# Kernel tuning notes

Measured on AMD Instinct MI355X. Metric: run time of the kernel, lower is better.

## Reference

```python
import jax, jax.numpy as jnp
import numpy as np

N_BITS = 8
IN_FEATURES = 2048
OUT_FEATURES = 512
BATCH = 8
THRESHOLD = 0.5


def setup_inputs() -> dict:
    key = jax.random.key(0)
    kx, kw = jax.random.split(key)
    x = jax.random.uniform(kx, (BATCH, IN_FEATURES), dtype=jnp.float32)
    # nn.init.normal_(weight, mean=0.5, std=1.0) then clamp_(0, 1)
    weight = 0.5 + jax.random.normal(kw, (IN_FEATURES, OUT_FEATURES * N_BITS), dtype=jnp.float32)
    weight = jnp.clip(weight, 0.0, 1.0)
    return {"x": x, "weight": weight}


def _carry_save_adder(addends):
    # addends: [M, F, n_bits] -> reduce over F via full-adder chain.
    # Bit index 0 = LSB; carry shifts one position toward MSB each step.
    M, F, nb = addends.shape
    a_seq = jnp.transpose(addends, (1, 0, 2))  # [F, M, nb]
    init = (jnp.zeros((M, nb), addends.dtype), jnp.zeros((M, nb), addends.dtype))

    def step(state, a):
        s, c = state
        t = s + a + c
        half = jnp.floor(t * 0.5)          # carry bit (zero-gradient)
        sum_b = t - 2.0 * half             # t mod 2 (identity gradient w.r.t. t)
        c_next = jnp.pad(half[:, :-1], ((0, 0), (1, 0)))  # shift-left: LSB carry-in = 0
        return (sum_b, c_next), None

    (s, c), _ = jax.lax.scan(step, init, a_seq)
    return s, c


def reference(x, weight):
    # STE binarization of the weights (forward value = hard bits)
    w = jnp.clip(weight, 0.0, 1.0)
    hard = w + jax.lax.stop_gradient((w >= THRESHOLD).astype(w.dtype) - w)
    # [B, F, 1] * [1, F, O*nb] -> [B, F, O*nb]
    ff = x[:, :, None] * hard[None, :, :]
    B, F, _ = ff.shape
    O = ff.shape[-1] // N_BITS
    # split(n_bits, dim=-1) + stack(dim=-3) + reshape -> [B*O, F, n_bits]
    stacked = ff.reshape(B, F, O, N_BITS).transpose(0, 2, 1, 3).reshape(B * O, F, N_BITS)
    s, carry = _carry_save_adder(stacked)   # [B*O, nb], [B*O, nb]
    s = s.reshape(B, N_BITS * O)
    return (s, carry)
```

## Files before the change

### kernel.cpp

```cpp
#include <hip/hip_runtime.h>


#define F_DIM 2048
#define K_DIM 4096
#define B_DIM 8
#define G     32
#define NG    (F_DIM / G)
#define NSB   (F_DIM / 64)

#define PK_BYTES (64 * NG * 64 * 4)

__device__ __forceinline__ float dpp_row_shr1(float v) {
    int r = __builtin_amdgcn_update_dpp(0, __float_as_int(v), 0x111, 0xf, 0xf, true);
    return __int_as_float(r);
}

__device__ __forceinline__ int sext_bit(unsigned bits, int u) {
#if __has_builtin(__builtin_amdgcn_sbfe)
    return __builtin_amdgcn_sbfe((int)bits, (unsigned)u, 1u);
#else
    return ((int)(bits << (31 - u))) >> 31;
#endif
}

__global__ __launch_bounds__(64) void pack_kernel(const float* __restrict__ w,
                                                  unsigned* __restrict__ pk) {
    const int lane = threadIdx.x;
    const int og   = blockIdx.x;
    const int f32  = blockIdx.y;
    const float* wp = w + og * 64 + lane;
    unsigned bits = 0;
#pragma unroll
    for (int j = 0; j < 32; ++j) {
        float wv = wp[(f32 * 32 + j) * K_DIM];
        bits |= (wv >= 0.5f ? 1u : 0u) << j;
    }
    pk[(og * 64 + f32) * 64 + lane] = bits;
}

__global__ __launch_bounds__(64, 1) void csa_main(const float* __restrict__ x,
                                                  const unsigned* __restrict__ pk,
                                                  float* __restrict__ out) {
    const int lane = threadIdx.x;
    const int og   = blockIdx.x + 8 * blockIdx.y;
    const int b    = blockIdx.z;
    const int k    = og * 64 + lane;

    const float kmask = ((lane & 7) == 7) ? 0.0f : 1.0f;

    const unsigned* bp = pk + og * (NG * 64) + lane;
    const int*      xp = (const int*)(x + b * F_DIM) + lane;

    unsigned pkA0 = bp[0 * 64], pkA1 = bp[1 * 64];
    int      xA   = xp[0 * 64];
    unsigned pkB0 = bp[2 * 64], pkB1 = bp[3 * 64];
    int      xB   = xp[1 * 64];

    float s = 0.0f;
    float h = 0.0f;

#define STEP64(PK0, PK1, XV)                                              \
    _Pragma("unroll")                                                      \
    for (int u = 0; u < 64; ++u) {                                         \
        int      xs   = __builtin_amdgcn_readlane((XV), u);                \
        unsigned bits = (u < 32) ? (PK0) : (PK1);                          \
        int      m    = sext_bit(bits, u & 31);                            \
        float    a    = __int_as_float(m & xs);     \
        float    cn   = dpp_row_shr1(h);           \
        float    uu   = s + a;                            \
        float    t    = uu + cn;                                           \
        bool     ge   = (t >= 2.0f);                                       \
        h = ge ? kmask : 0.0f;                                             \
        s = ge ? (t - 2.0f) : t;                                           \
    }

    for (int sb = 0; sb < NSB; sb += 2) {
        STEP64(pkA0, pkA1, xA);
        {
            int nsb = sb + 2; int csb = (nsb < NSB) ? nsb : (NSB - 2);
            pkA0 = bp[(2 * csb + 0) * 64];
            pkA1 = bp[(2 * csb + 1) * 64];
            xA   = xp[csb * 64];
        }
        STEP64(pkB0, pkB1, xB);
        {
            int nsb = sb + 3; int csb = (nsb < NSB) ? nsb : (NSB - 2);
            pkB0 = bp[(2 * csb + 0) * 64];
            pkB1 = bp[(2 * csb + 1) * 64];
            xB   = xp[csb * 64];
        }
    }
#undef STEP64

    float cfin = dpp_row_shr1(h);
    out[b * K_DIM + k]                 = s;
    out[B_DIM * K_DIM + b * K_DIM + k] = cfin;
}

#define U_FB  16
#define NB_FB 4
__global__ __launch_bounds__(64, 1) void csa_fallback(const float* __restrict__ x,
                                                      const float* __restrict__ weight,
                                                      float* __restrict__ out) {
    const int lane = threadIdx.x;
    const int og   = blockIdx.x + 8 * blockIdx.y;
    const int b    = blockIdx.z;
    const int k    = og * 64 + lane;
    const float kmask = ((lane & 7) == 7) ? 0.0f : 1.0f;
    int zero;
    asm volatile("v_mov_b32 %0, 0" : "=v"(zero));
    const float*  wp  = weight + k;
    const float4* xp4 = (const float4*)(x + b * F_DIM) + zero;
    float  wb[NB_FB][U_FB];
    float4 xb[NB_FB][U_FB / 4];
#pragma unroll
    for (int p = 0; p < NB_FB; ++p) {
#pragma unroll
        for (int u = 0; u < U_FB; ++u) wb[p][u] = wp[(p * U_FB + u) * K_DIM];
#pragma unroll
        for (int q = 0; q < U_FB / 4; ++q) xb[p][q] = xp4[(p * U_FB) / 4 + q];
    }
    float s = 0.0f, c = 0.0f;
    for (int f0 = 0; f0 < F_DIM; f0 += NB_FB * U_FB) {
#pragma unroll
        for (int p = 0; p < NB_FB; ++p) {
            const float* xf = (const float*)&xb[p][0];
#pragma unroll
            for (int u = 0; u < U_FB; ++u) {
                float a  = (wb[p][u] >= 0.5f) ? xf[u] : 0.0f;
                float uu = s + a;
                float t  = uu + c;
                bool  ge = (t >= 2.0f);
                float hh = ge ? kmask : 0.0f;
                s = ge ? (t - 2.0f) : t;
                c = dpp_row_shr1(hh);
            }
            int fb = f0 + p * U_FB + NB_FB * U_FB;
            int fc = (fb <= F_DIM - U_FB) ? fb : (F_DIM - U_FB);
#pragma unroll
            for (int u = 0; u < U_FB; ++u) wb[p][u] = wp[(fc + u) * K_DIM];
#pragma unroll
            for (int q = 0; q < U_FB / 4; ++q) xb[p][q] = xp4[fc / 4 + q];
        }
    }
    out[b * K_DIM + k]                 = s;
    out[B_DIM * K_DIM + b * K_DIM + k] = c;
}

extern "C" void kernel_launch(void* const* d_in, const int* in_sizes, int n_in,
                              void* d_out, int out_size, void* d_ws, size_t ws_size,
                              hipStream_t stream) {
    (void)in_sizes; (void)n_in; (void)out_size;
    const float* x      = (const float*)d_in[0];
    const float* weight = (const float*)d_in[1];
    float* out          = (float*)d_out;

    if (ws_size >= (size_t)PK_BYTES && d_ws != nullptr) {
        unsigned* pk = (unsigned*)d_ws;
        pack_kernel<<<dim3(64, 64, 1), dim3(64), 0, stream>>>(weight, pk);
        csa_main<<<dim3(8, 8, 8), dim3(64), 0, stream>>>(x, pk, out);
    } else {
        csa_fallback<<<dim3(8, 8, 8), dim3(64), 0, stream>>>(x, weight, out);
    }
}
```

Measured before the change: 114.4 us.

## Hand-schedule CSA step in inline asm with scalar x loads and software pipelining

Rewrites the inner carry-save step as inline GCN assembly. The carry shift is fused into a v_add_f32_dpp, and the compare/select is replaced by floor and fma. x values now come in as uniform 16-int vector loads into SGPRs instead of per-lane loads followed by readlane. The step is skewed so that each iteration computes the next addend and partial sum ahead of the dependent DPP add, which shortens the serial dependency chain. This relies on hand-managed DPP hazards and on the floor-based math matching the reference's mod-2 semantics; an out-of-range prefetch index is clamped at the tail.

```diff
diff --git a/kernel.cpp b/kernel.cpp
--- a/kernel.cpp
+++ b/kernel.cpp
@@ -4,11 +4,12 @@
 #define F_DIM 2048
 #define K_DIM 4096
 #define B_DIM 8
-#define G     32
-#define NG    (F_DIM / G)
+#define NG    (F_DIM / 32)
 #define NSB   (F_DIM / 64)
 
 #define PK_BYTES (64 * NG * 64 * 4)
+
+typedef int v16i __attribute__((ext_vector_type(16)));
 
 __device__ __forceinline__ float dpp_row_shr1(float v) {
     int r = __builtin_amdgcn_update_dpp(0, __float_as_int(v), 0x111, 0xf, 0xf, true);
@@ -38,6 +39,44 @@
     pk[(og * 64 + f32) * 64 + lane] = bits;
 }
 
+
+#define B(PKv, JLIT, XVAL) {                                                  \
+    const int xs_ = (XVAL);                                                   \
+    asm("v_add_f32_dpp %[t], %[h], %[uu] row_shr:1 row_mask:0xf bank_mask:0xf bound_ctrl:0\n\t" \
+        "v_mul_f32 %[g], 0.5, %[t]\n\t"                                       \
+        "v_floor_f32 %[c], %[g]\n\t"                                          \
+        "v_fma_f32 %[s], %[c], -2.0, %[t]\n\t"                                \
+        "v_mul_f32 %[h], %[c], %[km]\n\t"                                     \
+        "v_add_f32 %[uu], %[s], %[a]\n\t"                                     \
+        "v_bfe_i32 %[m], %[bits], " #JLIT ", 1\n\t"                           \
+        "v_and_b32 %[a], %[xs], %[m]"                                         \
+        : [t]"=&v"(t_), [g]"=&v"(g_), [c]"=&v"(c_), [m]"=&v"(m_),             \
+          [s]"+v"(s), [h]"+v"(h), [uu]"+v"(uu), [a]"+v"(a)                    \
+        : [bits]"v"(PKv), [xs]"s"(xs_), [km]"v"(km));                         \
+}
+
+#define SB64(P0, P1, PN, CQ, CQN) {                                           \
+    v16i q0 = xv[(CQ)+0], q1 = xv[(CQ)+1], q2 = xv[(CQ)+2], q3 = xv[(CQ)+3];  \
+    v16i qn = xv[(CQN)];                                                      \
+    B(P0, 2,q0[ 2]) B(P0, 3,q0[ 3]) B(P0, 4,q0[ 4]) B(P0, 5,q0[ 5])          \
+    B(P0, 6,q0[ 6]) B(P0, 7,q0[ 7]) B(P0, 8,q0[ 8]) B(P0, 9,q0[ 9])          \
+    B(P0,10,q0[10]) B(P0,11,q0[11]) B(P0,12,q0[12]) B(P0,13,q0[13])          \
+    B(P0,14,q0[14]) B(P0,15,q0[15])                                           \
+    B(P0,16,q1[ 0]) B(P0,17,q1[ 1]) B(P0,18,q1[ 2]) B(P0,19,q1[ 3])          \
+    B(P0,20,q1[ 4]) B(P0,21,q1[ 5]) B(P0,22,q1[ 6]) B(P0,23,q1[ 7])          \
+    B(P0,24,q1[ 8]) B(P0,25,q1[ 9]) B(P0,26,q1[10]) B(P0,27,q1[11])          \
+    B(P0,28,q1[12]) B(P0,29,q1[13]) B(P0,30,q1[14]) B(P0,31,q1[15])          \
+    B(P1, 0,q2[ 0]) B(P1, 1,q2[ 1]) B(P1, 2,q2[ 2]) B(P1, 3,q2[ 3])          \
+    B(P1, 4,q2[ 4]) B(P1, 5,q2[ 5]) B(P1, 6,q2[ 6]) B(P1, 7,q2[ 7])          \
+    B(P1, 8,q2[ 8]) B(P1, 9,q2[ 9]) B(P1,10,q2[10]) B(P1,11,q2[11])          \
+    B(P1,12,q2[12]) B(P1,13,q2[13]) B(P1,14,q2[14]) B(P1,15,q2[15])          \
+    B(P1,16,q3[ 0]) B(P1,17,q3[ 1]) B(P1,18,q3[ 2]) B(P1,19,q3[ 3])          \
+    B(P1,20,q3[ 4]) B(P1,21,q3[ 5]) B(P1,22,q3[ 6]) B(P1,23,q3[ 7])          \
+    B(P1,24,q3[ 8]) B(P1,25,q3[ 9]) B(P1,26,q3[10]) B(P1,27,q3[11])          \
+    B(P1,28,q3[12]) B(P1,29,q3[13]) B(P1,30,q3[14]) B(P1,31,q3[15])          \
+    B(PN, 0,qn[ 0]) B(PN, 1,qn[ 1])                                           \
+}
+
 __global__ __launch_bounds__(64, 1) void csa_main(const float* __restrict__ x,
                                                   const unsigned* __restrict__ pk,
                                                   float* __restrict__ out) {
@@ -46,56 +85,52 @@
     const int b    = blockIdx.z;
     const int k    = og * 64 + lane;
 
-    const float kmask = ((lane & 7) == 7) ? 0.0f : 1.0f;
+    const float kmf = ((lane & 7) == 7) ? 0.0f : 1.0f;
+    float km = kmf;
 
     const unsigned* bp = pk + og * (NG * 64) + lane;
-    const int*      xp = (const int*)(x + b * F_DIM) + lane;
-
-    unsigned pkA0 = bp[0 * 64], pkA1 = bp[1 * 64];
-    int      xA   = xp[0 * 64];
-    unsigned pkB0 = bp[2 * 64], pkB1 = bp[3 * 64];
-    int      xB   = xp[1 * 64];
-
-    float s = 0.0f;
-    float h = 0.0f;
-
-#define STEP64(PK0, PK1, XV)                                              \
-    _Pragma("unroll")                                                      \
-    for (int u = 0; u < 64; ++u) {                                         \
-        int      xs   = __builtin_amdgcn_readlane((XV), u);                \
-        unsigned bits = (u < 32) ? (PK0) : (PK1);                          \
-        int      m    = sext_bit(bits, u & 31);                            \
-        float    a    = __int_as_float(m & xs);     \
-        float    cn   = dpp_row_shr1(h);           \
-        float    uu   = s + a;                            \
-        float    t    = uu + cn;                                           \
-        bool     ge   = (t >= 2.0f);                                       \
-        h = ge ? kmask : 0.0f;                                             \
-        s = ge ? (t - 2.0f) : t;                                           \
-    }
-
+    const v16i*     xv = (const v16i*)(x + b * F_DIM);
+    const int*      xi = (const int*)(x + b * F_DIM);
+
+    unsigned pA0 = bp[0 * 64], pA1 = bp[1 * 64];
+    unsigned pB0 = bp[2 * 64], pB1 = bp[3 * 64];
+
+    int   xs0 = xi[0], xs1 = xi[1];
+    float a0  = __int_as_float(sext_bit(pA0, 0) & xs0);
+    float a   = __int_as_float(sext_bit(pA0, 1) & xs1);
+    float s = 0.0f, h, uu;
+    float t_, g_, c_;
+    int   m_;
+    asm("v_mov_b32 %[h], 0\n\t"
+        "v_add_f32 %[uu], 0, %[a0]\n\t"
+        "s_nop 1"
+        : [h]"=&v"(h), [uu]"=&v"(uu)
+        : [a0]"v"(a0));
+
+#pragma clang loop unroll(disable)
     for (int sb = 0; sb < NSB; sb += 2) {
-        STEP64(pkA0, pkA1, xA);
+        SB64(pA0, pA1, pB0, sb * 4, sb * 4 + 4);
         {
             int nsb = sb + 2; int csb = (nsb < NSB) ? nsb : (NSB - 2);
-            pkA0 = bp[(2 * csb + 0) * 64];
-            pkA1 = bp[(2 * csb + 1) * 64];
-            xA   = xp[csb * 64];
+            pA0 = bp[(2 * csb + 0) * 64];
+            pA1 = bp[(2 * csb + 1) * 64];
         }
-        STEP64(pkB0, pkB1, xB);
+        int cqn = (sb * 4 + 8 < 128) ? (sb * 4 + 8) : 127;
+        SB64(pB0, pB1, pA0, sb * 4 + 4, cqn);
         {
             int nsb = sb + 3; int csb = (nsb < NSB) ? nsb : (NSB - 2);
-            pkB0 = bp[(2 * csb + 0) * 64];
-            pkB1 = bp[(2 * csb + 1) * 64];
-            xB   = xp[csb * 64];
+            pB0 = bp[(2 * csb + 0) * 64];
+            pB1 = bp[(2 * csb + 1) * 64];
         }
     }
-#undef STEP64
 
     float cfin = dpp_row_shr1(h);
     out[b * K_DIM + k]                 = s;
     out[B_DIM * K_DIM + b * K_DIM + k] = cfin;
 }
+
+#undef SB64
+#undef B
 
 #define U_FB  16
 #define NB_FB 4
@@ -127,8 +162,8 @@
             const float* xf = (const float*)&xb[p][0];
 #pragma unroll
             for (int u = 0; u < U_FB; ++u) {
-                float a  = (wb[p][u] >= 0.5f) ? xf[u] : 0.0f;
-                float uu = s + a;
+                float av = (wb[p][u] >= 0.5f) ? xf[u] : 0.0f;
+                float uu = s + av;
                 float t  = uu + c;
                 bool  ge = (t >= 2.0f);
                 float hh = ge ? kmask : 0.0f;
```

Result: slower. 121.9 us (+6.5%).
